# Performance work log

Hardware: AMD Instinct MI355X
Metric: run time of the kernel (lower is better)

The kernel has to match this reference:

```python
import jax, jax.numpy as jnp
import numpy as np

B = 8          # batch
RES = 64       # resolution (H = W)
DIM = 512      # channels
HEADS = 8
HD = DIM // HEADS   # 64
HSP, WSP = RES, 8   # idx=0: H_sp=resolution, W_sp=split_size
NH, NW = RES // HSP, RES // WSP   # windows per axis


def setup_inputs() -> dict:
    key = jax.random.key(0)
    k1, k2, k3 = jax.random.split(key, 3)
    qkv = jax.random.normal(k1, (3, B, RES * RES, DIM), dtype=jnp.float32)
    lepe_w = jax.random.normal(k2, (DIM, 1, 3, 3), dtype=jnp.float32) * 0.1
    lepe_b = jax.random.normal(k3, (DIM,), dtype=jnp.float32) * 0.1
    return {"qkv": qkv, "lepe_w": lepe_w, "lepe_b": lepe_b}


def _to_windows(t):
    # [B, L, C] row-major -> [B*NH*NW, HSP*WSP, C]; equivalent to the
    # block-diagonal flex_attention mask grouping (y//H_sp, x//W_sp).
    t = t.reshape(B, NH, HSP, NW, WSP, DIM)
    return t.transpose(0, 1, 3, 2, 4, 5).reshape(B * NH * NW, HSP * WSP, DIM)


def _from_windows(t):
    t = t.reshape(B, NH, NW, HSP, WSP, DIM).transpose(0, 1, 3, 2, 4, 5)
    return t.reshape(B, RES * RES, DIM)


def reference(qkv, lepe_w, lepe_b):
    q, k, v = qkv[0], qkv[1], qkv[2]            # each [B, L, C]
    qw, kw, vw = _to_windows(q), _to_windows(k), _to_windows(v)

    # LePE: depthwise 3x3 conv on v laid out per-window as [n, C, HSP, WSP]
    vimg = vw.transpose(0, 2, 1).reshape(-1, DIM, HSP, WSP)
    lepe = jax.lax.conv_general_dilated(
        vimg, lepe_w, window_strides=(1, 1), padding='SAME',
        dimension_numbers=('NCHW', 'OIHW', 'NCHW'), feature_group_count=DIM)
    lepe = lepe + lepe_b[None, :, None, None]
    lepe = lepe.reshape(-1, DIM, HSP * WSP).transpose(0, 2, 1)  # [n, T, C]

    def split_heads(t):
        return t.reshape(t.shape[0], t.shape[1], HEADS, HD)

    qh, kh, vh, lh = map(split_heads, (qw, kw, vw, lepe))
    scale = 1.0 / np.sqrt(HD).astype(np.float32)  # flex_attention default scale
    scores = jnp.einsum('wqhd,wkhd->whqk', qh, kh) * scale
    attn = jax.nn.softmax(scores, axis=-1)
    out = jnp.einsum('whqk,wkhd->wqhd', attn, vh) + lh   # [n, T, H, hd]
    out = out.reshape(out.shape[0], out.shape[1], DIM)
    return _from_windows(out)
```

## Files before the change

### kernel.cpp

```cpp
#include <hip/hip_runtime.h>
#include <hip/hip_bf16.h>

#define DIMV 512
#define HDV  64
#define KRING_B 16384
#define VT_BASE KRING_B
#define SMEM_B (VT_BASE + 65536)

typedef __bf16 bf16x8_t __attribute__((ext_vector_type(8)));
typedef float f32x4_t __attribute__((ext_vector_type(4)));

union Frag { bf16x8_t v; unsigned short u[8]; unsigned int w[4]; uint2 d[2]; uint4 q; };

static __device__ __forceinline__ unsigned short f2bf(float f) {
  return __builtin_bit_cast(unsigned short, (__bf16)f);
}
static __device__ __forceinline__ float bf2f(unsigned int h) {
  return __builtin_bit_cast(float, h << 16);
}
static __device__ __forceinline__ uint2 pack4(const float4 f) {
  uint2 r;
  r.x = (unsigned)f2bf(f.x) | ((unsigned)f2bf(f.y) << 16);
  r.y = (unsigned)f2bf(f.z) | ((unsigned)f2bf(f.w) << 16);
  return r;
}

#define BARRIER_NODRAIN() asm volatile("s_waitcnt lgkmcnt(0)\n\ts_barrier" ::: "memory")

__global__ __launch_bounds__(1024, 4)
void lepe_attn_kernel(const float* __restrict__ qkv,
                      const float* __restrict__ lw,
                      const float* __restrict__ lb,
                      float* __restrict__ out)
{
  __shared__ __align__(16) unsigned char smem[SMEM_B];

  const int head = blockIdx.x & 7;
  const int win  = blockIdx.x >> 3;
  const int bat  = win >> 3;
  const int nw   = win & 7;

  const int tid  = threadIdx.x;
  const int wave = tid >> 6, lane = tid & 63;
  const int l15  = lane & 15, g = lane >> 4;

  const float* qptr = qkv;
  const float* kptr = qkv + 16777216;
  const float* vptr = qkv + 33554432;
  const int rowbase = bat * 4096;

  auto grow = [&](int tok) -> int {
    return rowbase + ((tok >> 3) << 6) + (nw << 3) + (tok & 7);
  };

  const int s_t = tid >> 4;
  const int s_c = (tid & 15) * 4;
  const size_t GSTRIDE = 262144;
  const float* kg = kptr + (size_t)grow(s_t) * DIMV + head * HDV + s_c;
  const float* vg = vptr + (size_t)grow(s_t) * DIMV + head * HDV + s_c;

  const int lr  = s_t & 31;
  const int kwb = (s_t >> 5) * 4096 + (lr >> 4) * 2048 + (s_c >> 5) * 1024
                + ((lr & 15) + 16 * ((s_c >> 3) & 3)) * 16 + (s_c & 7) * 2;

  float4 kc4;
  auto issueK = [&](int c) { kc4 = *(const float4*)(kg + (size_t)c * GSTRIDE); };
  auto writeK = [&](int c) {
    *(uint2*)(smem + (c & 1) * 8192 + kwb) = pack4(kc4);
  };

  issueK(0);
  float4 vin[8];
  #pragma unroll
  for (int j = 0; j < 8; ++j) vin[j] = *(const float4*)(vg + (size_t)j * GSTRIDE);

  const float QSC = 0.1803368801f;
  const int qbase = wave * 32;
  float4 qin[8];
  #pragma unroll
  for (int qi = 0; qi < 2; ++qi) {
    const float* qp = qptr + (size_t)grow(qbase + qi * 16 + l15) * DIMV + head * HDV;
    #pragma unroll
    for (int kc = 0; kc < 2; ++kc) {
      qin[qi * 4 + kc * 2 + 0] = *(const float4*)(qp + kc * 32 + 8 * g);
      qin[qi * 4 + kc * 2 + 1] = *(const float4*)(qp + kc * 32 + 8 * g + 4);
    }
  }

  writeK(0);
  #pragma unroll
  for (int j = 0; j < 8; ++j) {
    const int t2 = 2 * (j * 64 + s_t);
    float fv[4] = {vin[j].x, vin[j].y, vin[j].z, vin[j].w};
    #pragma unroll
    for (int i = 0; i < 4; ++i) {
      const int d = s_c + i;
      *(unsigned short*)(smem + VT_BASE + d * 1024 + (t2 ^ ((d & 7) << 4))) = f2bf(fv[i]);
    }
  }

  Frag qf[2][2];
  #pragma unroll
  for (int qi = 0; qi < 2; ++qi)
    #pragma unroll
    for (int kc = 0; kc < 2; ++kc) {
      const float4 f0 = qin[qi * 4 + kc * 2 + 0];
      const float4 f1 = qin[qi * 4 + kc * 2 + 1];
      qf[qi][kc].u[0] = f2bf(f0.x * QSC); qf[qi][kc].u[1] = f2bf(f0.y * QSC);
      qf[qi][kc].u[2] = f2bf(f0.z * QSC); qf[qi][kc].u[3] = f2bf(f0.w * QSC);
      qf[qi][kc].u[4] = f2bf(f1.x * QSC); qf[qi][kc].u[5] = f2bf(f1.y * QSC);
      qf[qi][kc].u[6] = f2bf(f1.z * QSC); qf[qi][kc].u[7] = f2bf(f1.w * QSC);
    }

  __syncthreads();

  const f32x4_t zero4 = {0.f, 0.f, 0.f, 0.f};
  f32x4_t ot[4][2];
  #pragma unroll
  for (int di = 0; di < 4; ++di)
    #pragma unroll
    for (int qi = 0; qi < 2; ++qi) ot[di][qi] = zero4;
  float lsum[2] = {0.f, 0.f};

  const int vswz = (l15 & 7) << 4;

  for (int c = 0; c < 8; ++c) {
    if (c < 7) issueK(c + 1);

    #pragma unroll
    for (int t2i = 0; t2i < 2; ++t2i) {
      const int kt = c * 2 + t2i;
      const unsigned char* kbase = smem + (c & 1) * 8192 + t2i * 4096 + lane * 16;

      Frag kf[2][2];
      #pragma unroll
      for (int ki = 0; ki < 2; ++ki)
        #pragma unroll
        for (int kc = 0; kc < 2; ++kc)
          kf[ki][kc].q = *(const uint4*)(kbase + ki * 2048 + kc * 1024);

      f32x4_t st[2][2];
      #pragma unroll
      for (int ki = 0; ki < 2; ++ki)
        #pragma unroll
        for (int qi = 0; qi < 2; ++qi) st[ki][qi] = zero4;

      __builtin_amdgcn_s_setprio(1);
      #pragma unroll
      for (int kc = 0; kc < 2; ++kc)
        #pragma unroll
        for (int ki = 0; ki < 2; ++ki)
          #pragma unroll
          for (int qi = 0; qi < 2; ++qi)
            st[ki][qi] = __builtin_amdgcn_mfma_f32_16x16x32_bf16(
                kf[ki][kc].v, qf[qi][kc].v, st[ki][qi], 0, 0, 0);
      __builtin_amdgcn_s_setprio(0);

      #pragma unroll
      for (int ki = 0; ki < 2; ++ki)
        #pragma unroll
        for (int qi = 0; qi < 2; ++qi) {
          f32x4_t s = st[ki][qi];
          #pragma unroll
          for (int r = 0; r < 4; ++r) {
            float pr = __builtin_amdgcn_exp2f(s[r]);
            s[r] = pr;
            lsum[qi] += pr;
          }
          st[ki][qi] = s;
        }

      Frag vf[4];
      #pragma unroll
      for (int di = 0; di < 4; ++di) {
        const unsigned char* vrow = smem + VT_BASE + (di * 16 + l15) * 1024;
        vf[di].d[0] = *(const uint2*)(vrow + ((kt * 64 + 8 * g) ^ vswz));
        vf[di].d[1] = *(const uint2*)(vrow + ((kt * 64 + 32 + 8 * g) ^ vswz));
      }

      __builtin_amdgcn_s_setprio(1);
      #pragma unroll
      for (int qi = 0; qi < 2; ++qi) {
        Frag pb;
        #pragma unroll
        for (int r = 0; r < 4; ++r) {
          pb.u[r]     = f2bf(st[0][qi][r]);
          pb.u[4 + r] = f2bf(st[1][qi][r]);
        }
        #pragma unroll
        for (int di = 0; di < 4; ++di)
          ot[di][qi] = __builtin_amdgcn_mfma_f32_16x16x32_bf16(
              vf[di].v, pb.v, ot[di][qi], 0, 0, 0);
      }
      __builtin_amdgcn_s_setprio(0);
    }

    if (c < 7) { writeK(c + 1); BARRIER_NODRAIN(); }
  }

  float rl[2];
  #pragma unroll
  for (int qi = 0; qi < 2; ++qi) {
    float s = lsum[qi];
    s += __shfl_xor(s, 16, 64);
    s += __shfl_xor(s, 32, 64);
    rl[qi] = 1.0f / s;
  }

  float lout[32];
  {
    float wgt[9];
    const float* wp = lw + (size_t)(head * HDV + lane) * 9;
    #pragma unroll
    for (int i = 0; i < 9; ++i) wgt[i] = wp[i];
    const float bias = lb[head * HDV + lane];
    const int yb = wave * 4;
    const unsigned char* vrow = smem + VT_BASE + lane * 1024;
    const int lsw = (lane & 7) << 4;

    float rm[8], rc[8], rp2[8];
    auto loadrow = [&](int y, float* dst) {
      if ((unsigned)y < 64u) {
        uint4 a = *(const uint4*)(vrow + ((y * 16) ^ lsw));
        dst[0] = bf2f(a.x & 0xffffu); dst[1] = bf2f(a.x >> 16);
        dst[2] = bf2f(a.y & 0xffffu); dst[3] = bf2f(a.y >> 16);
        dst[4] = bf2f(a.z & 0xffffu); dst[5] = bf2f(a.z >> 16);
        dst[6] = bf2f(a.w & 0xffffu); dst[7] = bf2f(a.w >> 16);
      } else {
        #pragma unroll
        for (int x = 0; x < 8; ++x) dst[x] = 0.f;
      }
    };
    loadrow(yb - 1, rm);
    loadrow(yb, rc);
    #pragma unroll
    for (int yy = 0; yy < 4; ++yy) {
      loadrow(yb + yy + 1, rp2);
      #pragma unroll
      for (int x = 0; x < 8; ++x) {
        float acc = bias;
        if (x > 0) acc += rm[x-1]*wgt[0] + rc[x-1]*wgt[3] + rp2[x-1]*wgt[6];
        acc += rm[x]*wgt[1] + rc[x]*wgt[4] + rp2[x]*wgt[7];
        if (x < 7) acc += rm[x+1]*wgt[2] + rc[x+1]*wgt[5] + rp2[x+1]*wgt[8];
        lout[yy * 8 + x] = acc;
      }
      #pragma unroll
      for (int x = 0; x < 8; ++x) { rm[x] = rc[x]; rc[x] = rp2[x]; }
    }
  }

  BARRIER_NODRAIN();

  #pragma unroll
  for (int t = 0; t < 32; ++t) {
    const int tok = qbase + t;
    *(unsigned short*)(smem + VT_BASE + tok * 128 + ((2 * lane) ^ ((tok & 7) << 4)))
        = f2bf(lout[t]);
  }
  BARRIER_NODRAIN();

  #pragma unroll
  for (int qi = 0; qi < 2; ++qi) {
    const float rlq = rl[qi];
    const int tok = qbase + qi * 16 + l15;
    const unsigned char* brow = smem + VT_BASE + tok * 128;
    const int bsw = (l15 & 7) << 4;
    float* op = out + (size_t)grow(tok) * DIMV + head * HDV;
    #pragma unroll
    for (int di = 0; di < 4; ++di) {
      uint2 lv = *(const uint2*)(brow + ((di * 32 + 8 * g) ^ bsw));
      float4 o;
      o.x = ot[di][qi][0] * rlq + bf2f(lv.x & 0xffffu);
      o.y = ot[di][qi][1] * rlq + bf2f(lv.x >> 16);
      o.z = ot[di][qi][2] * rlq + bf2f(lv.y & 0xffffu);
      o.w = ot[di][qi][3] * rlq + bf2f(lv.y >> 16);
      *(float4*)(op + di * 16 + 4 * g) = o;
    }
  }
}

extern "C" void kernel_launch(void* const* d_in, const int* in_sizes, int n_in,
                              void* d_out, int out_size, void* d_ws, size_t ws_size,
                              hipStream_t stream) {
  const float* qkv = (const float*)d_in[0];
  const float* lw  = (const float*)d_in[1];
  const float* lb  = (const float*)d_in[2];
  float* out = (float*)d_out;
  (void)in_sizes; (void)n_in; (void)out_size; (void)d_ws; (void)ws_size;

  dim3 grid(512);
  dim3 block(1024);
  hipLaunchKernelGGL(lepe_attn_kernel, grid, block, 0, stream, qkv, lw, lb, out);
}
```

Baseline: 83.93 us.

## Stream V alongside K in double-buffered chunks instead of loading V upfront

V is no longer loaded in full before the attention loop. K and V are now fetched together in four larger chunks, each covering two 64-token groups, and written into shared memory one chunk ahead of use, so the V loads overlap with the MFMA work. The K ring buffer doubles in size, which makes total shared memory 96KB, and launch bounds drop from 4 to 2 blocks per CU. That frees more registers but lowers the possible occupancy and adds per-iteration global loads.

```diff
diff --git a/kernel.cpp b/kernel.cpp
--- a/kernel.cpp
+++ b/kernel.cpp
@@ -3,7 +3,7 @@
 
 #define DIMV 512
 #define HDV  64
-#define KRING_B 16384
+#define KRING_B 32768
 #define VT_BASE KRING_B
 #define SMEM_B (VT_BASE + 65536)
 
@@ -27,7 +27,7 @@
 
 #define BARRIER_NODRAIN() asm volatile("s_waitcnt lgkmcnt(0)\n\ts_barrier" ::: "memory")
 
-__global__ __launch_bounds__(1024, 4)
+__global__ __launch_bounds__(1024, 2)
 void lepe_attn_kernel(const float* __restrict__ qkv,
                       const float* __restrict__ lw,
                       const float* __restrict__ lb,
@@ -59,20 +59,35 @@
   const float* kg = kptr + (size_t)grow(s_t) * DIMV + head * HDV + s_c;
   const float* vg = vptr + (size_t)grow(s_t) * DIMV + head * HDV + s_c;
 
-  const int lr  = s_t & 31;
-  const int kwb = (s_t >> 5) * 4096 + (lr >> 4) * 2048 + (s_c >> 5) * 1024
-                + ((lr & 15) + 16 * ((s_c >> 3) & 3)) * 16 + (s_c & 7) * 2;
-
-  float4 kc4;
-  auto issueK = [&](int c) { kc4 = *(const float4*)(kg + (size_t)c * GSTRIDE); };
-  auto writeK = [&](int c) {
-    *(uint2*)(smem + (c & 1) * 8192 + kwb) = pack4(kc4);
+  const int lr   = s_t & 31;
+  const int kwb0 = (s_t >> 5) * 4096 + (lr >> 4) * 2048 + (s_c >> 5) * 1024
+                 + ((lr & 15) + 16 * ((s_c >> 3) & 3)) * 16 + (s_c & 7) * 2;
+
+  float4 ck0, ck1, cv0, cv1;
+  auto issueC = [&](int c) {
+    ck0 = *(const float4*)(kg + (size_t)(2 * c) * GSTRIDE);
+    ck1 = *(const float4*)(kg + (size_t)(2 * c + 1) * GSTRIDE);
+    cv0 = *(const float4*)(vg + (size_t)(2 * c) * GSTRIDE);
+    cv1 = *(const float4*)(vg + (size_t)(2 * c + 1) * GSTRIDE);
   };
-
-  issueK(0);
-  float4 vin[8];
-  #pragma unroll
-  for (int j = 0; j < 8; ++j) vin[j] = *(const float4*)(vg + (size_t)j * GSTRIDE);
+  auto writeC = [&](int c) {
+    unsigned char* slot = smem + (c & 1) * 16384;
+    *(uint2*)(slot + kwb0)        = pack4(ck0);
+    *(uint2*)(slot + 8192 + kwb0) = pack4(ck1);
+    #pragma unroll
+    for (int gi = 0; gi < 2; ++gi) {
+      const float4 vv = gi ? cv1 : cv0;
+      const int t2 = 2 * ((2 * c + gi) * 64 + s_t);
+      float fv[4] = {vv.x, vv.y, vv.z, vv.w};
+      #pragma unroll
+      for (int i = 0; i < 4; ++i) {
+        const int d = s_c + i;
+        *(unsigned short*)(smem + VT_BASE + d * 1024 + (t2 ^ ((d & 7) << 4))) = f2bf(fv[i]);
+      }
+    }
+  };
+
+  issueC(0);
 
   const float QSC = 0.1803368801f;
   const int qbase = wave * 32;
@@ -87,17 +102,7 @@
     }
   }
 
-  writeK(0);
-  #pragma unroll
-  for (int j = 0; j < 8; ++j) {
-    const int t2 = 2 * (j * 64 + s_t);
-    float fv[4] = {vin[j].x, vin[j].y, vin[j].z, vin[j].w};
-    #pragma unroll
-    for (int i = 0; i < 4; ++i) {
-      const int d = s_c + i;
-      *(unsigned short*)(smem + VT_BASE + d * 1024 + (t2 ^ ((d & 7) << 4))) = f2bf(fv[i]);
-    }
-  }
+  writeC(0);
 
   Frag qf[2][2];
   #pragma unroll
@@ -124,13 +129,14 @@
 
   const int vswz = (l15 & 7) << 4;
 
-  for (int c = 0; c < 8; ++c) {
-    if (c < 7) issueK(c + 1);
-
-    #pragma unroll
-    for (int t2i = 0; t2i < 2; ++t2i) {
-      const int kt = c * 2 + t2i;
-      const unsigned char* kbase = smem + (c & 1) * 8192 + t2i * 4096 + lane * 16;
+  #pragma unroll
+  for (int c = 0; c < 4; ++c) {
+    if (c < 3) issueC(c + 1);
+
+    #pragma unroll
+    for (int t4 = 0; t4 < 4; ++t4) {
+      const int kt = c * 4 + t4;
+      const unsigned char* kbase = smem + (c & 1) * 16384 + t4 * 4096 + lane * 16;
 
       Frag kf[2][2];
       #pragma unroll
@@ -195,7 +201,7 @@
       __builtin_amdgcn_s_setprio(0);
     }
 
-    if (c < 7) { writeK(c + 1); BARRIER_NODRAIN(); }
+    if (c < 3) { writeC(c + 1); BARRIER_NODRAIN(); }
   }
 
   float rl[2];
```

New measurement: 85.48 us. No clear change (+1.9%).
